# Kernel optimization log

Hardware: AMD Instinct MI355X
Metric: run time of the kernel (lower is better)

Reference implementation:

```python
import jax, jax.numpy as jnp
import numpy as np

KS = 2       # kernel_size (pad (0,1,0,1)+unfold only tiles to HxW for k=2)
L = 2        # num_attn_blocks
NH = 4       # n_heads
C = 128      # latent_dim
DH = C // NH
SCALE = 1.0 / float(np.sqrt(DH))


def _ln(x, eps=1e-6):
    m = jnp.mean(x, axis=-1, keepdims=True)
    v = jnp.var(x, axis=-1, keepdims=True)
    return (x - m) * jax.lax.rsqrt(v + eps)


def setup_inputs() -> dict:
    key = jax.random.key(0)
    ks = jax.random.split(key, 24)
    B, Hd, Wd, upf = 2, 64, 96, 2
    d = {
        'feat_map': jax.random.normal(ks[0], (B, C, Hd, Wd), jnp.float32),
        'feat_map_up': jax.random.normal(ks[1], (B, C, Hd * upf, Wd * upf), jnp.float32),
    }
    shapes = {'ctx_ln_b': (L, C), 'q_w': (L, C, C), 'q_b': (L, C), 'k_w': (L, C, C), 'k_b': (L, C),
              'v_w': (L, C, C), 'v_b': (L, C), 'o_w': (L, C, C), 'o_b': (L, C),
              'fc1_w': (L, C, 4 * C), 'fc1_b': (L, 4 * C), 'fc2_w': (L, 4 * C, C), 'fc2_b': (L, C),
              'out1_w': (3 * C, 3 * C), 'out1_b': (3 * C,), 'out2_w': (3 * C, 1), 'out2_b': (1,)}
    for i, (n, shp) in enumerate(shapes.items()):
        d[n] = jax.random.normal(ks[2 + i], shp, jnp.float32) * 0.02
    d['ctx_ln_g'] = jnp.ones((L, C), jnp.float32)
    d['upsample_factor'] = 2
    return d


def _forward(feat_map, feat_map_up, ctx_ln_g, ctx_ln_b, q_w, q_b, k_w, k_b, v_w, v_b,
             o_w, o_b, fc1_w, fc1_b, fc2_w, fc2_b, out1_w, out1_b, out2_w, out2_b, upf):
    B, _, Hd, Wd = feat_map.shape
    Hu, Wu = Hd * upf, Wd * upf
    N, K2 = B * Hu * Wu, KS * KS
    rh = jnp.minimum((jnp.arange(Hu) // upf)[:, None] + jnp.arange(KS)[None, :], Hd - 1)  # (Hu,KS)
    rw = jnp.minimum((jnp.arange(Wu) // upf)[:, None] + jnp.arange(KS)[None, :], Wd - 1)  # (Wu,KS)
    ctx = feat_map[:, :, rh][:, :, :, :, rw]                      # (B,C,Hu,KS,Wu,KS)
    ctx = jnp.transpose(ctx, (0, 2, 4, 3, 5, 1)).reshape(N, K2, C)  # (N,K2,C)
    # ALiBi bias: -L1(|up pixel coord - upf*down window coord|), separable in y/x
    dy = -jnp.abs(jnp.arange(Hu)[:, None] - rh * upf).astype(jnp.float32)  # (Hu,KS)
    dx = -jnp.abs(jnp.arange(Wu)[:, None] - rw * upf).astype(jnp.float32)  # (Wu,KS)
    cd = (dy[:, None, :, None] + dx[None, :, None, :]).reshape(Hu * Wu, K2)
    cd = jnp.tile(cd, (B, 1))                                     # (N,K2)
    x24 = 24.0 ** (1.0 / NH)
    slopes = 1.0 / x24 ** (jnp.arange(NH, dtype=jnp.float32) + 1.0)
    bias = slopes[None, :, None, None] * cd[:, None, None, :]     # (N,NH,1,K2)

    x = jnp.transpose(feat_map_up, (0, 2, 3, 1)).reshape(N, 1, C)
    for l in range(L):
        xn = _ln(x)
        cn = _ln(ctx, eps=1e-5) * ctx_ln_g[l] + ctx_ln_b[l]
        q = (xn @ q_w[l] + q_b[l]).reshape(N, 1, NH, DH).transpose(0, 2, 1, 3)
        k = (cn @ k_w[l] + k_b[l]).reshape(N, K2, NH, DH).transpose(0, 2, 1, 3)
        v = (cn @ v_w[l] + v_b[l]).reshape(N, K2, NH, DH).transpose(0, 2, 1, 3)
        sim = jnp.einsum('nhqd,nhkd->nhqk', q, k) * SCALE + bias
        attn = jax.nn.softmax(sim, axis=-1)
        o = jnp.einsum('nhqk,nhkd->nhqd', attn, v).transpose(0, 2, 1, 3).reshape(N, 1, C)
        x = x + o @ o_w[l] + o_b[l]
        h = _ln(x)
        x = x + jax.nn.gelu(h @ fc1_w[l] + fc1_b[l], approximate=True) @ fc2_w[l] + fc2_b[l]

    xf = _ln(x)      # (N,1,C)
    cf = _ln(ctx)    # (N,K2,C)
    fin = jnp.concatenate([jnp.broadcast_to(xf, (N, K2, C)), cf, xf - cf], axis=-1)  # (N,K2,3C)
    h1 = jax.nn.gelu(fin @ out1_w + out1_b, approximate=False)
    out = (h1 @ out2_w + out2_b).reshape(B, Hu, Wu, K2).transpose(0, 3, 1, 2)  # (B,K2,Hu,Wu)
    return jax.nn.softmax(out, axis=1)


def reference(feat_map, feat_map_up, ctx_ln_b, q_w, q_b, k_w, k_b, v_w, v_b, o_w, o_b,
              fc1_w, fc1_b, fc2_w, fc2_b, out1_w, out1_b, out2_w, out2_b, ctx_ln_g,
              upsample_factor):
    return _forward(feat_map, feat_map_up, ctx_ln_g, ctx_ln_b, q_w, q_b, k_w, k_b,
                    v_w, v_b, o_w, o_b, fc1_w, fc1_b, fc2_w, fc2_b,
                    out1_w, out1_b, out2_w, out2_b, upsample_factor)
```

## Files before the change

kernel.cpp:

```cpp
#include <hip/hip_runtime.h>
#include <math.h>

#define C_   128
#define HU_  128
#define WU_  192
#define HD_  64
#define WD_  96
#define HWD_ (HD_ * WD_)

typedef unsigned short u16;
typedef __attribute__((ext_vector_type(8))) short s8v;
typedef __attribute__((ext_vector_type(4))) float f4v;

#define OFF_Q   0
#define OFF_K   32768
#define OFF_V   65536
#define OFF_O   98304
#define OFF_F1  131072
#define OFF_F2  262144
#define OFF_XC  393216
#define OFF_CC  442368
#define OFF_NRM 491520
#define OFF_VB  2064384

#define SLOT 2176

__device__ __forceinline__ u16 f2bf(float f) {
    unsigned u = __float_as_uint(f);
    unsigned r = (u + 0x7FFFu + ((u >> 16) & 1u)) >> 16;
    return (u16)r;
}
__device__ __forceinline__ float bfu(u16 h) { return __uint_as_float(((unsigned)h) << 16); }

__device__ __forceinline__ float gelu_tanh(float x) {
    float u = 1.5957691216057308f * (x + 0.044715f * x * x * x);
    float e = __expf(u);
    float th = 1.0f - 2.0f / (1.0f + e);
    return 0.5f * x * (1.0f + th);
}
__device__ __forceinline__ float fast_erf(float x) {
    float z = fabsf(x);
    float t = 1.0f / (1.0f + 0.3275911f * z);
    float p = t * (0.254829592f + t * (-0.284496736f + t * (1.421413741f +
              t * (-1.453152027f + t * 1.061405429f))));
    float r = 1.0f - p * __expf(-z * z);
    return copysignf(r, x);
}
__device__ __forceinline__ float gelu_erf(float x) {
    return 0.5f * x * (1.0f + fast_erf(x * 0.7071067811865476f));
}

__device__ __forceinline__ void glds1(const u16* src, u16* dst, int lane) {
    __builtin_amdgcn_global_load_lds(
        (const __attribute__((address_space(1))) void*)(src + (size_t)lane * 8),
        (__attribute__((address_space(3))) void*)dst, 16, 0, 0);
}
#define GW4() do { asm volatile("s_waitcnt vmcnt(4)" ::: "memory"); __builtin_amdgcn_s_barrier(); } while (0)
#define GW3() do { asm volatile("s_waitcnt vmcnt(3)" ::: "memory"); __builtin_amdgcn_s_barrier(); } while (0)
#define GW0() do { asm volatile("s_waitcnt vmcnt(0)" ::: "memory"); __builtin_amdgcn_s_barrier(); } while (0)
#define BAR() __builtin_amdgcn_s_barrier()
#define WFENCE() asm volatile("s_waitcnt lgkmcnt(0)" ::: "memory")

__global__ __launch_bounds__(256) void swz_all(
    const float* __restrict__ q_w, const float* __restrict__ k_w,
    const float* __restrict__ v_w, const float* __restrict__ o_w,
    const float* __restrict__ f1w, const float* __restrict__ f2w,
    const float* __restrict__ o1w,
    const float* __restrict__ ctx_g, const float* __restrict__ ctx_b,
    const float* __restrict__ vb_in, u16* __restrict__ ws)
{
    int tid = blockIdx.x * 256 + threadIdx.x;
    int f = tid >> 6, lane = tid & 63;
    if (f >= 964) return;
    if (f >= 960) {
        int lf = f - 960;
        int ly = lf >> 1, col = (lf & 1) * 64 + lane;
        float s = vb_in[ly * 128 + col];
        const float* bp = ctx_b + ly * 128;
        const float* wp = v_w + (size_t)ly * 128 * 128 + col;
        for (int c = 0; c < 128; ++c) s += bp[c] * wp[(size_t)c * 128];
        ((float*)(ws + OFF_VB))[ly * 128 + col] = s;
        return;
    }
    int rq = 8 * (lane >> 4), cq = lane & 15;
    const float* src; const float* src2 = nullptr; float sgn = 1.f;
    int NT, N, dstoff, lf;
    bool scale_g = false;
    if (f < 64)       { src = q_w;  NT = 8;  N = 128; dstoff = OFF_Q;  lf = f; }
    else if (f < 128) { src = k_w;  NT = 8;  N = 128; dstoff = OFF_K;  lf = f - 64;  scale_g = true; }
    else if (f < 192) { src = v_w;  NT = 8;  N = 128; dstoff = OFF_V;  lf = f - 128; scale_g = true; }
    else if (f < 256) { src = o_w;  NT = 8;  N = 128; dstoff = OFF_O;  lf = f - 192; }
    else if (f < 512) { src = f1w;  NT = 32; N = 512; dstoff = OFF_F1; lf = f - 256; }
    else if (f < 768) { src = f2w;  NT = 8;  N = 128; dstoff = OFF_F2; lf = f - 512; }
    else if (f < 864) { src = o1w;             src2 = o1w + 256 * 384; sgn =  1.f;
                        NT = 24; N = 384; dstoff = OFF_XC; lf = f - 768; }
    else              { src = o1w + 128 * 384; src2 = o1w + 256 * 384; sgn = -1.f;
                        NT = 24; N = 384; dstoff = OFF_CC; lf = f - 864; }
    int kt = lf / NT, nt = lf - kt * NT;
    int row0 = kt * 32 + rq, col = nt * 16 + cq;
    s8v o;
#pragma unroll
    for (int j = 0; j < 8; ++j) {
        float v = src[(size_t)(row0 + j) * N + col];
        if (src2) v += sgn * src2[(size_t)(row0 + j) * N + col];
        if (scale_g) v *= ctx_g[row0 + j];
        o[j] = (short)f2bf(v);
    }
    *(s8v*)(ws + dstoff + (size_t)lf * 512 + (size_t)lane * 8) = o;
}

__global__ __launch_bounds__(256) void norm_kernel(const float* __restrict__ fm,
                                                   u16* __restrict__ dst) {
    int row = blockIdx.x;
    int b = row >> 6, y = row & 63;
    __shared__ float tile[128 * 97];
    __shared__ float smean[96], srst[96];
    for (int idx = threadIdx.x; idx < 128 * 96; idx += 256) {
        int c = idx / 96, w = idx - c * 96;
        tile[c * 97 + w] = fm[(((size_t)b * 128 + c) * 64 + y) * 96 + w];
    }
    __syncthreads();
    if (threadIdx.x < 96) {
        int w = threadIdx.x;
        float s = 0.f, ss = 0.f;
        for (int c = 0; c < 128; ++c) { float v = tile[c * 97 + w]; s += v; ss += v * v; }
        float mn = s * (1.f / 128.f);
        smean[w] = mn;
        srst[w]  = rsqrtf(ss * (1.f / 128.f) - mn * mn + 1e-5f);
    }
    __syncthreads();
    for (int idx = threadIdx.x; idx < 96 * 16; idx += 256) {
        int w = idx >> 4, cg = idx & 15;
        float mn = smean[w], iv = srst[w];
        s8v o;
#pragma unroll
        for (int j = 0; j < 8; ++j)
            o[j] = (short)f2bf((tile[(8 * cg + j) * 97 + w] - mn) * iv);
        *(s8v*)(dst + ((size_t)row * 96 + w) * 128 + 8 * cg) = o;
    }
}

__global__ __launch_bounds__(128, 2) void fused_kernel(
    const u16*  __restrict__ nrmb, const float* __restrict__ fmu,
    const u16*  __restrict__ wsb,
    const float* __restrict__ qb, const float* __restrict__ ob,
    const float* __restrict__ f1b, const float* __restrict__ f2b,
    const float* __restrict__ o1b, const float* __restrict__ o2w,
    const float* __restrict__ o2b,
    float* __restrict__ out)
{
    const int tid  = threadIdx.x;
    const int wid  = tid >> 6;
    const int lane = tid & 63;
    const int cidx = lane & 15, quad = lane >> 4;
    const int n0 = blockIdx.x * 32 + wid * 16;
    const int b  = n0 / (HU_ * WU_);
    const int rem = n0 - b * (HU_ * WU_);
    const int hu  = rem / WU_;
    const int wu0 = rem - hu * WU_;

    __shared__ __align__(16) u16 wlds[2][4096];
    __shared__ __align__(16) u16 arena2[2][2 * SLOT];
    __shared__ float s_at2[2][272];
    u16*   const arena = arena2[wid];
    float* const s_at  = s_at2[wid];
    float* const s_rs  = s_at;

    const float* vbp = (const float*)(wsb + OFF_VB);

    float xacc[8][4];
#pragma unroll
    for (int nt = 0; nt < 8; ++nt) {
        int ch = 16 * nt + cidx;
        float4 v = *(const float4*)(fmu + ((size_t)(b * C_ + ch) * HU_ + hu) * WU_ + wu0 + 4 * quad);
        xacc[nt][0] = v.x; xacc[nt][1] = v.y; xacc[nt][2] = v.z; xacc[nt][3] = v.w;
    }

    const float slopes[4] = {0.451801007f, 0.204124145f, 0.092223264f, 0.041666668f};
    const int ry0 = min(hu >> 1, HD_ - 1);
    const int ry1 = min((hu >> 1) + 1, HD_ - 1);
    const float dyv0 = -(float)abs(hu - 2 * ry0);
    const float dyv1 = -(float)abs(hu - 2 * ry1);

    const int k2l = cidx & 3;
    const int ryl = (k2l >> 1) ? ry1 : ry0;
    int cbase[4];
#pragma unroll
    for (int mt = 0; mt < 4; ++mt) {
        int p = 4 * mt + (cidx >> 2);
        int rxv = min(((wu0 + p) >> 1) + (k2l & 1), WD_ - 1);
        cbase[mt] = ((b * HD_ + ryl) * WD_ + rxv) * 128;
    }

#pragma unroll 1
    for (int ly = 0; ly < 2; ++ly) {
        const u16* Wq = wsb + OFF_Q  + ly * 16384;
        const u16* Wk = wsb + OFF_K  + ly * 16384;
        const u16* Wv = wsb + OFF_V  + ly * 16384;
        const u16* Wo = wsb + OFF_O  + ly * 16384;
        const u16* W1 = wsb + OFF_F1 + ly * 65536;
        const u16* W2 = wsb + OFF_F2 + ly * 65536;

        s8v fr[4][2];

#pragma unroll
        for (int jl = 0; jl < 4; ++jl) {
            int j = 4 * wid + jl;
            glds1(Wq + (size_t)j * 512, &wlds[0][j * 512], lane);
        }
#pragma unroll
        for (int jl = 0; jl < 4; ++jl) {
            int j = 4 * wid + jl;
            glds1(Wq + (size_t)(8 + j) * 512, &wlds[1][j * 512], lane);
        }

        {
            float mo[4], io[4];
#pragma unroll
            for (int r = 0; r < 4; ++r) {
                float s = 0.f, ss = 0.f;
#pragma unroll
                for (int nt = 0; nt < 8; ++nt) { float v = xacc[nt][r]; s += v; ss += v * v; }
#pragma unroll
                for (int m = 1; m <= 8; m <<= 1) { s += __shfl_xor(s, m, 64); ss += __shfl_xor(ss, m, 64); }
                float mn = s * (1.f / 128.f);
                mo[r] = mn; io[r] = rsqrtf(ss * (1.f / 128.f) - mn * mn + 1e-6f);
            }
#pragma unroll
            for (int nt = 0; nt < 8; ++nt)
#pragma unroll
                for (int r = 0; r < 4; ++r)
                    arena[(4 * quad + r) * 136 + 16 * nt + cidx] =
                        f2bf((xacc[nt][r] - mo[r]) * io[r]);
        }
        WFENCE();
        s8v a_xn[4];
#pragma unroll
        for (int kt = 0; kt < 4; ++kt)
            a_xn[kt] = *(const s8v*)(arena + cidx * 136 + kt * 32 + 8 * quad);

        {
            f4v qa[8];
#pragma unroll
            for (int nt = 0; nt < 8; ++nt) {
                float bvv = qb[ly * C_ + 16 * nt + cidx];
                f4v t = {bvv, bvv, bvv, bvv}; qa[nt] = t;
            }
#pragma unroll
            for (int g = 0; g < 4; ++g) {
                if (g < 3) { GW4(); } else { GW0(); }
#pragma unroll
                for (int nt = 0; nt < 8; ++nt) {
                    s8v w = *(const s8v*)&wlds[g & 1][nt * 512 + lane * 8];
                    qa[nt] = __builtin_amdgcn_mfma_f32_16x16x32_bf16(a_xn[g], w, qa[nt], 0, 0, 0);
                }
                BAR();
                if (g < 2) {
#pragma unroll
                    for (int jl = 0; jl < 4; ++jl) {
                        int j = 4 * wid + jl;
                        glds1(Wq + (size_t)((g + 2) * 8 + j) * 512, &wlds[g & 1][j * 512], lane);
                    }
                }
            }
#pragma unroll
            for (int kt = 0; kt < 4; ++kt)
#pragma unroll
                for (int i = 0; i < 2; ++i)
                    fr[kt][i] = *(const s8v*)(nrmb + cbase[i] + kt * 32 + 8 * quad);
#pragma unroll
            for (int jl = 0; jl < 4; ++jl) {
                int j = 4 * wid + jl;
                glds1(Wk + (size_t)(((j & 3) * 8) + (j >> 2)) * 512, &wlds[0][j * 512], lane);
            }
#pragma unroll
            for (int jl = 0; jl < 4; ++jl) {
                int j = 4 * wid + jl;
                int jc = 8 + j;
                glds1(Wk + (size_t)(((jc & 3) * 8) + (jc >> 2)) * 512, &wlds[1][j * 512], lane);
            }
#pragma unroll
            for (int nt = 0; nt < 8; ++nt)
#pragma unroll
                for (int r = 0; r < 4; ++r)
                    arena[(4 * quad + r) * 136 + 16 * nt + cidx] = f2bf(qa[nt][r]);
        }
        WFENCE();

#pragma unroll
        for (int g = 0; g < 8; ++g) {
            if (g < 7) { GW4(); } else { GW0(); }
            if (g == 4) {
#pragma unroll
                for (int kt = 0; kt < 4; ++kt)
#pragma unroll
                    for (int i = 0; i < 2; ++i)
                        fr[kt][i] = *(const s8v*)(nrmb + cbase[2 + i] + kt * 32 + 8 * quad);
            }
            const int mh = g >> 2, h = g & 3;
            float part[2][4];
#pragma unroll
            for (int i = 0; i < 2; ++i)
#pragma unroll
                for (int r = 0; r < 4; ++r) part[i][r] = 0.f;
#pragma unroll
            for (int ntp = 0; ntp < 2; ++ntp) {
                const int nt = 2 * h + ntp;
                f4v ka[2];
#pragma unroll
                for (int i = 0; i < 2; ++i) { f4v t = {0.f, 0.f, 0.f, 0.f}; ka[i] = t; }
#pragma unroll
                for (int kt = 0; kt < 4; ++kt) {
                    s8v w = *(const s8v*)&wlds[g & 1][(ntp * 4 + kt) * 512 + lane * 8];
                    ka[0] = __builtin_amdgcn_mfma_f32_16x16x32_bf16(fr[kt][0], w, ka[0], 0, 0, 0);
                    ka[1] = __builtin_amdgcn_mfma_f32_16x16x32_bf16(fr[kt][1], w, ka[1], 0, 0, 0);
                }
#pragma unroll
                for (int i = 0; i < 2; ++i) {
                    float qv = bfu(arena[(4 * (2 * mh + i) + quad) * 136 + 16 * nt + cidx]);
#pragma unroll
                    for (int r = 0; r < 4; ++r) part[i][r] = fmaf(qv, ka[i][r], part[i][r]);
                }
            }
#pragma unroll
            for (int i = 0; i < 2; ++i)
#pragma unroll
                for (int r = 0; r < 4; ++r) {
#pragma unroll
                    for (int m = 1; m <= 8; m <<= 1) part[i][r] += __shfl_xor(part[i][r], m, 64);
                }
            if (cidx == 0) {
#pragma unroll
                for (int i = 0; i < 2; ++i) {
                    float4 t = {part[i][0], part[i][1], part[i][2], part[i][3]};
                    *(float4*)&s_at[(4 * (2 * mh + i) + quad) * 16 + 4 * h] = t;
                }
            }
            BAR();
            if (g < 6) {
                const int gn = g + 2;
#pragma unroll
                for (int jl = 0; jl < 4; ++jl) {
                    int j = 4 * wid + jl;
                    int jc = 8 * (gn & 3) + j;
                    glds1(Wk + (size_t)(((jc & 3) * 8) + (jc >> 2)) * 512, &wlds[g & 1][j * 512], lane);
                }
            }
        }
#pragma unroll
        for (int kt = 0; kt < 4; ++kt)
#pragma unroll
            for (int i = 0; i < 2; ++i)
                fr[kt][i] = *(const s8v*)(nrmb + cbase[i] + kt * 32 + 8 * quad);
#pragma unroll
        for (int jl = 0; jl < 4; ++jl) {
            int j = 4 * wid + jl;
            glds1(Wv + (size_t)(((j & 3) * 8) + (j >> 2)) * 512, &wlds[0][j * 512], lane);
        }
#pragma unroll
        for (int jl = 0; jl < 4; ++jl) {
            int j = 4 * wid + jl;
            glds1(Wv + (size_t)(((j & 3) * 8) + 2 + (j >> 2)) * 512, &wlds[1][j * 512], lane);
        }
        WFENCE();

        {
            int p = lane >> 2, h = lane & 3;
            float4 sc = *(float4*)&s_at[p * 16 + 4 * h];
            int pw = wu0 + p;
            float sim[4] = {sc.x, sc.y, sc.z, sc.w};
#pragma unroll
            for (int r = 0; r < 4; ++r) {
                int rxv = min((pw >> 1) + (r & 1), WD_ - 1);
                float cd = ((r >> 1) ? dyv1 : dyv0) - (float)abs(pw - 2 * rxv);
                sim[r] = sim[r] * 0.17677669529663687f + slopes[h] * cd;
            }
            float mx = fmaxf(fmaxf(sim[0], sim[1]), fmaxf(sim[2], sim[3]));
            float e0 = __expf(sim[0] - mx), e1 = __expf(sim[1] - mx);
            float e2 = __expf(sim[2] - mx), e3 = __expf(sim[3] - mx);
            float si = 1.f / (e0 + e1 + e2 + e3);
            float4 at = {e0 * si, e1 * si, e2 * si, e3 * si};
            *(float4*)&s_at[p * 16 + 4 * h] = at;
        }
        WFENCE();

#pragma unroll
        for (int g = 0; g < 8; ++g) {
            if (g < 7) { GW4(); } else { GW0(); }
            if (g == 4) {
#pragma unroll
                for (int kt = 0; kt < 4; ++kt)
#pragma unroll
                    for (int i = 0; i < 2; ++i)
                        fr[kt][i] = *(const s8v*)(nrmb + cbase[2 + i] + kt * 32 + 8 * quad);
            }
            const int mh = g >> 2, gp = g & 3;
#pragma unroll
            for (int ntp = 0; ntp < 2; ++ntp) {
                const int nt = 2 * gp + ntp;
                float vbb = vbp[ly * C_ + 16 * nt + cidx];
                f4v va[2];
#pragma unroll
                for (int i = 0; i < 2; ++i) { f4v t = {vbb, vbb, vbb, vbb}; va[i] = t; }
#pragma unroll
                for (int kt = 0; kt < 4; ++kt) {
                    s8v w = *(const s8v*)&wlds[g & 1][(ntp * 4 + kt) * 512 + lane * 8];
                    va[0] = __builtin_amdgcn_mfma_f32_16x16x32_bf16(fr[kt][0], w, va[0], 0, 0, 0);
                    va[1] = __builtin_amdgcn_mfma_f32_16x16x32_bf16(fr[kt][1], w, va[1], 0, 0, 0);
                }
                const int h = nt >> 1;
#pragma unroll
                for (int i = 0; i < 2; ++i) {
                    const int mt = 2 * mh + i;
                    float4 at = *(float4*)&s_at[(4 * mt + quad) * 16 + 4 * h];
                    float ov = at.x * va[i][0] + at.y * va[i][1] + at.z * va[i][2] + at.w * va[i][3];
                    arena[(4 * mt + quad) * 136 + 16 * nt + cidx] = f2bf(ov);
                }
            }
            BAR();
            if (g < 6) {
                const int gq = (g + 2) & 3;
#pragma unroll
                for (int jl = 0; jl < 4; ++jl) {
                    int j = 4 * wid + jl;
                    glds1(Wv + (size_t)(((j & 3) * 8) + 2 * gq + (j >> 2)) * 512, &wlds[g & 1][j * 512], lane);
                }
            }
        }
#pragma unroll
        for (int jl = 0; jl < 4; ++jl) {
            int j = 4 * wid + jl;
            glds1(Wo + (size_t)j * 512, &wlds[0][j * 512], lane);
        }
#pragma unroll
        for (int jl = 0; jl < 4; ++jl) {
            int j = 4 * wid + jl;
            glds1(Wo + (size_t)(8 + j) * 512, &wlds[1][j * 512], lane);
        }
        WFENCE();

        {
            s8v a_o[4];
#pragma unroll
            for (int kt = 0; kt < 4; ++kt)
                a_o[kt] = *(const s8v*)(arena + cidx * 136 + kt * 32 + 8 * quad);
            f4v oa[8];
#pragma unroll
            for (int nt = 0; nt < 8; ++nt) {
                float bvv = ob[ly * C_ + 16 * nt + cidx];
                f4v t = {bvv, bvv, bvv, bvv}; oa[nt] = t;
            }
#pragma unroll
            for (int g = 0; g < 4; ++g) {
                if (g < 3) { GW4(); } else { GW0(); }
#pragma unroll
                for (int nt = 0; nt < 8; ++nt) {
                    s8v w = *(const s8v*)&wlds[g & 1][nt * 512 + lane * 8];
                    oa[nt] = __builtin_amdgcn_mfma_f32_16x16x32_bf16(a_o[g], w, oa[nt], 0, 0, 0);
                }
                BAR();
                if (g < 2) {
#pragma unroll
                    for (int jl = 0; jl < 4; ++jl) {
                        int j = 4 * wid + jl;
                        glds1(Wo + (size_t)((g + 2) * 8 + j) * 512, &wlds[g & 1][j * 512], lane);
                    }
                }
            }
#pragma unroll
            for (int jl = 0; jl < 4; ++jl) {
                int j = 4 * wid + jl;
                glds1(W1 + (size_t)j * 512, &wlds[0][j * 512], lane);
            }
#pragma unroll
            for (int jl = 0; jl < 4; ++jl) {
                int j = 4 * wid + jl;
                glds1(W1 + (size_t)(32 + j) * 512, &wlds[1][j * 512], lane);
            }
#pragma unroll
            for (int nt = 0; nt < 8; ++nt)
#pragma unroll
                for (int r = 0; r < 4; ++r) xacc[nt][r] += oa[nt][r];
        }

        {
            float mo[4], io[4];
#pragma unroll
            for (int r = 0; r < 4; ++r) {
                float s = 0.f, ss = 0.f;
#pragma unroll
                for (int nt = 0; nt < 8; ++nt) { float v = xacc[nt][r]; s += v; ss += v * v; }
#pragma unroll
                for (int m = 1; m <= 8; m <<= 1) { s += __shfl_xor(s, m, 64); ss += __shfl_xor(ss, m, 64); }
                float mn = s * (1.f / 128.f);
                mo[r] = mn; io[r] = rsqrtf(ss * (1.f / 128.f) - mn * mn + 1e-6f);
            }
#pragma unroll
            for (int nt = 0; nt < 8; ++nt)
#pragma unroll
                for (int r = 0; r < 4; ++r)
                    arena[(4 * quad + r) * 136 + 16 * nt + cidx] =
                        f2bf((xacc[nt][r] - mo[r]) * io[r]);
        }
        WFENCE();
        s8v a_hn[4];
#pragma unroll
        for (int kt = 0; kt < 4; ++kt)
            a_hn[kt] = *(const s8v*)(arena + cidx * 136 + kt * 32 + 8 * quad);

        {
            f4v ga[8];
#pragma unroll
            for (int nt = 0; nt < 8; ++nt) {
                float bvv = f2b[ly * C_ + 16 * nt + cidx];
                f4v t = {bvv, bvv, bvv, bvv}; ga[nt] = t;
            }
#pragma unroll 1
            for (int c = 0; c < 4; ++c) {
                f4v fa[8];
#pragma unroll
                for (int nt = 0; nt < 8; ++nt) {
                    float bvv = f1b[ly * 512 + 128 * c + 16 * nt + cidx];
                    f4v t = {bvv, bvv, bvv, bvv}; fa[nt] = t;
                }
#pragma unroll
                for (int g = 0; g < 4; ++g) {
                    if (g < 3) { GW4(); } else { GW0(); }
#pragma unroll
                    for (int nt = 0; nt < 8; ++nt) {
                        s8v w = *(const s8v*)&wlds[g & 1][nt * 512 + lane * 8];
                        fa[nt] = __builtin_amdgcn_mfma_f32_16x16x32_bf16(a_hn[g], w, fa[nt], 0, 0, 0);
                    }
                    BAR();
                    if (g < 2) {
#pragma unroll
                        for (int jl = 0; jl < 4; ++jl) {
                            int j = 4 * wid + jl;
                            glds1(W1 + (size_t)((g + 2) * 32 + 8 * c + j) * 512, &wlds[g & 1][j * 512], lane);
                        }
                    }
                }
#pragma unroll
                for (int jl = 0; jl < 4; ++jl) {
                    int j = 4 * wid + jl;
                    glds1(W2 + (size_t)(32 * c + j) * 512, &wlds[0][j * 512], lane);
                }
#pragma unroll
                for (int jl = 0; jl < 4; ++jl) {
                    int j = 4 * wid + jl;
                    glds1(W2 + (size_t)(32 * c + 8 + j) * 512, &wlds[1][j * 512], lane);
                }
#pragma unroll
                for (int nt = 0; nt < 8; ++nt)
#pragma unroll
                    for (int r = 0; r < 4; ++r)
                        arena[SLOT + (4 * quad + r) * 136 + 16 * nt + cidx] =
                            f2bf(gelu_tanh(fa[nt][r]));
                WFENCE();
#pragma unroll
                for (int g = 0; g < 4; ++g) {
                    if (g < 3) { GW4(); } else { GW0(); }
                    s8v a = *(const s8v*)(arena + SLOT + cidx * 136 + g * 32 + 8 * quad);
#pragma unroll
                    for (int nt = 0; nt < 8; ++nt) {
                        s8v w = *(const s8v*)&wlds[g & 1][nt * 512 + lane * 8];
                        ga[nt] = __builtin_amdgcn_mfma_f32_16x16x32_bf16(a, w, ga[nt], 0, 0, 0);
                    }
                    BAR();
                    if (g < 2) {
#pragma unroll
                        for (int jl = 0; jl < 4; ++jl) {
                            int j = 4 * wid + jl;
                            glds1(W2 + (size_t)(32 * c + (g + 2) * 8 + j) * 512, &wlds[g & 1][j * 512], lane);
                        }
                    }
                }
                if (c < 3) {
#pragma unroll
                    for (int jl = 0; jl < 4; ++jl) {
                        int j = 4 * wid + jl;
                        glds1(W1 + (size_t)(8 * (c + 1) + j) * 512, &wlds[0][j * 512], lane);
                    }
#pragma unroll
                    for (int jl = 0; jl < 4; ++jl) {
                        int j = 4 * wid + jl;
                        glds1(W1 + (size_t)(32 + 8 * (c + 1) + j) * 512, &wlds[1][j * 512], lane);
                    }
                }
            }
#pragma unroll
            for (int nt = 0; nt < 8; ++nt)
#pragma unroll
                for (int r = 0; r < 4; ++r) xacc[nt][r] += ga[nt][r];
        }
    }

    const u16* Wxc = wsb + OFF_XC;
    const u16* Wcc = wsb + OFF_CC;
#pragma unroll
    for (int jl = 0; jl < 3; ++jl) {
        int j = 3 * wid + jl;
        glds1(Wxc + (size_t)((j / 3) * 24 + (j % 3)) * 512, &wlds[0][j * 512], lane);
    }
#pragma unroll
    for (int jl = 0; jl < 3; ++jl) {
        int j = 3 * wid + jl;
        glds1(Wxc + (size_t)((2 + j / 3) * 24 + (j % 3)) * 512, &wlds[1][j * 512], lane);
    }
    {
        float mo[4], io[4];
#pragma unroll
        for (int r = 0; r < 4; ++r) {
            float s = 0.f, ss = 0.f;
#pragma unroll
            for (int nt = 0; nt < 8; ++nt) { float v = xacc[nt][r]; s += v; ss += v * v; }
#pragma unroll
            for (int m = 1; m <= 8; m <<= 1) { s += __shfl_xor(s, m, 64); ss += __shfl_xor(ss, m, 64); }
            float mn = s * (1.f / 128.f);
            mo[r] = mn; io[r] = rsqrtf(ss * (1.f / 128.f) - mn * mn + 1e-6f);
        }
#pragma unroll
        for (int nt = 0; nt < 8; ++nt)
#pragma unroll
            for (int r = 0; r < 4; ++r)
                arena[(4 * quad + r) * 136 + 16 * nt + cidx] =
                    f2bf((xacc[nt][r] - mo[r]) * io[r]);
    }
    WFENCE();
    s8v a_xf[4];
#pragma unroll
    for (int kt = 0; kt < 4; ++kt)
        a_xf[kt] = *(const s8v*)(arena + cidx * 136 + kt * 32 + 8 * quad);

    float part[4][4];
#pragma unroll
    for (int mt = 0; mt < 4; ++mt)
#pragma unroll
        for (int r = 0; r < 4; ++r) part[mt][r] = 0.f;

#pragma unroll 1
    for (int it = 0; it < 8; ++it) {
        const int nbase = 6 * (it >> 1) + 3 * (it & 1);
        {
            f4v hx[3];
#pragma unroll
            for (int ntl = 0; ntl < 3; ++ntl) {
                float hb = o1b[16 * (nbase + ntl) + cidx];
                f4v t = {hb, hb, hb, hb}; hx[ntl] = t;
            }
            GW3();
#pragma unroll
            for (int kt = 0; kt < 2; ++kt)
#pragma unroll
                for (int ntl = 0; ntl < 3; ++ntl) {
                    s8v w = *(const s8v*)&wlds[0][(kt * 3 + ntl) * 512 + lane * 8];
                    hx[ntl] = __builtin_amdgcn_mfma_f32_16x16x32_bf16(a_xf[kt], w, hx[ntl], 0, 0, 0);
                }
            GW0();
#pragma unroll
            for (int kt = 2; kt < 4; ++kt)
#pragma unroll
                for (int ntl = 0; ntl < 3; ++ntl) {
                    s8v w = *(const s8v*)&wlds[1][((kt - 2) * 3 + ntl) * 512 + lane * 8];
                    hx[ntl] = __builtin_amdgcn_mfma_f32_16x16x32_bf16(a_xf[kt], w, hx[ntl], 0, 0, 0);
                }
            BAR();
            if (it < 7) {
                const int nb2 = 6 * ((it + 1) >> 1) + 3 * ((it + 1) & 1);
#pragma unroll
                for (int jl = 0; jl < 3; ++jl) {
                    int j = 3 * wid + jl;
                    glds1(Wxc + (size_t)((j / 3) * 24 + nb2 + (j % 3)) * 512, &wlds[0][j * 512], lane);
                }
#pragma unroll
                for (int jl = 0; jl < 3; ++jl) {
                    int j = 3 * wid + jl;
                    glds1(Wxc + (size_t)((2 + j / 3) * 24 + nb2 + (j % 3)) * 512, &wlds[1][j * 512], lane);
                }
            }
#pragma unroll
            for (int ntl = 0; ntl < 3; ++ntl)
#pragma unroll
                for (int r = 0; r < 4; ++r)
                    arena[SLOT + (4 * quad + r) * 56 + 16 * ntl + cidx] = f2bf(hx[ntl][r]);
        }
        WFENCE();

        f4v hc[3][4];
#pragma unroll
        for (int ntl = 0; ntl < 3; ++ntl)
#pragma unroll
            for (int mt = 0; mt < 4; ++mt) { f4v t = {0.f, 0.f, 0.f, 0.f}; hc[ntl][mt] = t; }
#pragma unroll 1
        for (int kt = 0; kt < 4; ++kt) {
            s8v frh[4];
#pragma unroll
            for (int mt = 0; mt < 4; ++mt)
                frh[mt] = *(const s8v*)(nrmb + cbase[mt] + kt * 32 + 8 * quad);
#pragma unroll
            for (int ntl = 0; ntl < 3; ++ntl) {
                s8v w = *(const s8v*)(Wcc + ((size_t)((kt * 24 + nbase + ntl) * 64 + lane)) * 8);
#pragma unroll
                for (int mt = 0; mt < 4; ++mt)
                    hc[ntl][mt] = __builtin_amdgcn_mfma_f32_16x16x32_bf16(frh[mt], w, hc[ntl][mt], 0, 0, 0);
            }
        }

#pragma unroll
        for (int ntl = 0; ntl < 3; ++ntl) {
            float w2v = o2w[16 * (nbase + ntl) + cidx];
#pragma unroll
            for (int mt = 0; mt < 4; ++mt)
#pragma unroll
                for (int r = 0; r < 4; ++r) {
                    float h1 = hc[ntl][mt][r] +
                               bfu(arena[SLOT + (4 * mt + quad) * 56 + 16 * ntl + cidx]);
                    part[mt][r] = fmaf(gelu_erf(h1), w2v, part[mt][r]);
                }
        }
        WFENCE();
    }

#pragma unroll
    for (int mt = 0; mt < 4; ++mt)
#pragma unroll
        for (int r = 0; r < 4; ++r) {
#pragma unroll
            for (int m = 1; m <= 8; m <<= 1) part[mt][r] += __shfl_xor(part[mt][r], m, 64);
            part[mt][r] += o2b[0];
        }
    if (cidx == 0) {
#pragma unroll
        for (int mt = 0; mt < 4; ++mt) {
            float4 t = {part[mt][0], part[mt][1], part[mt][2], part[mt][3]};
            *(float4*)&s_rs[(4 * mt + quad) * 4] = t;
        }
    }
    WFENCE();

    if (lane < 16) {
        int p = lane;
        float4 vv = *(float4*)&s_rs[4 * p];
        float mx = fmaxf(fmaxf(vv.x, vv.y), fmaxf(vv.z, vv.w));
        float e0 = __expf(vv.x - mx), e1 = __expf(vv.y - mx);
        float e2 = __expf(vv.z - mx), e3 = __expf(vv.w - mx);
        float si = 1.f / (e0 + e1 + e2 + e3);
        size_t base = ((size_t)(b * 4) * HU_ + hu) * WU_ + wu0 + p;
        out[base]                          = e0 * si;
        out[base + (size_t)HU_ * WU_]      = e1 * si;
        out[base + (size_t)2 * HU_ * WU_]  = e2 * si;
        out[base + (size_t)3 * HU_ * WU_]  = e3 * si;
    }
}

extern "C" void kernel_launch(void* const* d_in, const int* in_sizes, int n_in,
                              void* d_out, int out_size, void* d_ws, size_t ws_size,
                              hipStream_t stream) {
    const float* feat_map    = (const float*)d_in[0];
    const float* feat_map_up = (const float*)d_in[1];
    const float* ctx_ln_b    = (const float*)d_in[2];
    const float* q_w  = (const float*)d_in[3];
    const float* q_b  = (const float*)d_in[4];
    const float* k_w  = (const float*)d_in[5];
    const float* v_w  = (const float*)d_in[7];
    const float* v_b  = (const float*)d_in[8];
    const float* o_w  = (const float*)d_in[9];
    const float* o_b  = (const float*)d_in[10];
    const float* fc1_w = (const float*)d_in[11];
    const float* fc1_b = (const float*)d_in[12];
    const float* fc2_w = (const float*)d_in[13];
    const float* fc2_b = (const float*)d_in[14];
    const float* out1_w = (const float*)d_in[15];
    const float* out1_b = (const float*)d_in[16];
    const float* out2_w = (const float*)d_in[17];
    const float* out2_b = (const float*)d_in[18];
    const float* ctx_ln_g = (const float*)d_in[19];
    float* out = (float*)d_out;
    u16* ws = (u16*)d_ws;

    swz_all<<<242, 256, 0, stream>>>(q_w, k_w, v_w, o_w, fc1_w, fc2_w, out1_w,
                                     ctx_ln_g, ctx_ln_b, v_b, ws);
    norm_kernel<<<128, 256, 0, stream>>>(feat_map, ws + OFF_NRM);

    fused_kernel<<<1536, 128, 0, stream>>>(
        ws + OFF_NRM, feat_map_up, ws,
        q_b, o_b, fc1_b, fc2_b,
        out1_b, out2_w, out2_b, out);
}
```

Measured before the change: 412.6 us.

## Widen fused kernel to four waves per block sharing LDS weight tiles

The fused kernel moves from 2 to 4 waves per block (256 threads, half as many blocks), so each weight chunk staged through global_load_lds is shared by 64 rows instead of 32. Each wave now issues half as many async loads per chunk, and the vmcnt waits are adjusted to match. The per-wave attention scratch is folded into the arena to save LDS, and the reload of the second half of the context fragments is moved earlier in the K/V loops. In exchange, barriers now synchronise four waves, which can add stall time, and register pressure under launch_bounds(256,2) may limit occupancy.

```diff
diff --git a/kernel.cpp b/kernel.cpp
--- a/kernel.cpp
+++ b/kernel.cpp
@@ -55,8 +55,7 @@
         (const __attribute__((address_space(1))) void*)(src + (size_t)lane * 8),
         (__attribute__((address_space(3))) void*)dst, 16, 0, 0);
 }
-#define GW4() do { asm volatile("s_waitcnt vmcnt(4)" ::: "memory"); __builtin_amdgcn_s_barrier(); } while (0)
-#define GW3() do { asm volatile("s_waitcnt vmcnt(3)" ::: "memory"); __builtin_amdgcn_s_barrier(); } while (0)
+#define GW2() do { asm volatile("s_waitcnt vmcnt(2)" ::: "memory"); __builtin_amdgcn_s_barrier(); } while (0)
 #define GW0() do { asm volatile("s_waitcnt vmcnt(0)" ::: "memory"); __builtin_amdgcn_s_barrier(); } while (0)
 #define BAR() __builtin_amdgcn_s_barrier()
 #define WFENCE() asm volatile("s_waitcnt lgkmcnt(0)" ::: "memory")
@@ -140,7 +139,7 @@
     }
 }
 
-__global__ __launch_bounds__(128, 2) void fused_kernel(
+__global__ __launch_bounds__(256, 2) void fused_kernel(
     const u16*  __restrict__ nrmb, const float* __restrict__ fmu,
     const u16*  __restrict__ wsb,
     const float* __restrict__ qb, const float* __restrict__ ob,
@@ -153,17 +152,16 @@
     const int wid  = tid >> 6;
     const int lane = tid & 63;
     const int cidx = lane & 15, quad = lane >> 4;
-    const int n0 = blockIdx.x * 32 + wid * 16;
+    const int n0 = blockIdx.x * 64 + wid * 16;
     const int b  = n0 / (HU_ * WU_);
     const int rem = n0 - b * (HU_ * WU_);
     const int hu  = rem / WU_;
     const int wu0 = rem - hu * WU_;
 
     __shared__ __align__(16) u16 wlds[2][4096];
-    __shared__ __align__(16) u16 arena2[2][2 * SLOT];
-    __shared__ float s_at2[2][272];
+    __shared__ __align__(16) u16 arena2[4][2 * SLOT];
     u16*   const arena = arena2[wid];
-    float* const s_at  = s_at2[wid];
+    float* const s_at  = (float*)(arena + SLOT + 1024);
     float* const s_rs  = s_at;
 
     const float* vbp = (const float*)(wsb + OFF_VB);
@@ -204,13 +202,13 @@
         s8v fr[4][2];
 
 #pragma unroll
-        for (int jl = 0; jl < 4; ++jl) {
-            int j = 4 * wid + jl;
+        for (int jl = 0; jl < 2; ++jl) {
+            int j = 2 * wid + jl;
             glds1(Wq + (size_t)j * 512, &wlds[0][j * 512], lane);
         }
 #pragma unroll
-        for (int jl = 0; jl < 4; ++jl) {
-            int j = 4 * wid + jl;
+        for (int jl = 0; jl < 2; ++jl) {
+            int j = 2 * wid + jl;
             glds1(Wq + (size_t)(8 + j) * 512, &wlds[1][j * 512], lane);
         }
 
@@ -248,7 +246,7 @@
             }
 #pragma unroll
             for (int g = 0; g < 4; ++g) {
-                if (g < 3) { GW4(); } else { GW0(); }
+                if (g < 3) { GW2(); } else { GW0(); }
 #pragma unroll
                 for (int nt = 0; nt < 8; ++nt) {
                     s8v w = *(const s8v*)&wlds[g & 1][nt * 512 + lane * 8];
@@ -257,8 +255,8 @@
                 BAR();
                 if (g < 2) {
 #pragma unroll
-                    for (int jl = 0; jl < 4; ++jl) {
-                        int j = 4 * wid + jl;
+                    for (int jl = 0; jl < 2; ++jl) {
+                        int j = 2 * wid + jl;
                         glds1(Wq + (size_t)((g + 2) * 8 + j) * 512, &wlds[g & 1][j * 512], lane);
                     }
                 }
@@ -269,13 +267,13 @@
                 for (int i = 0; i < 2; ++i)
                     fr[kt][i] = *(const s8v*)(nrmb + cbase[i] + kt * 32 + 8 * quad);
 #pragma unroll
-            for (int jl = 0; jl < 4; ++jl) {
-                int j = 4 * wid + jl;
+            for (int jl = 0; jl < 2; ++jl) {
+                int j = 2 * wid + jl;
                 glds1(Wk + (size_t)(((j & 3) * 8) + (j >> 2)) * 512, &wlds[0][j * 512], lane);
             }
 #pragma unroll
-            for (int jl = 0; jl < 4; ++jl) {
-                int j = 4 * wid + jl;
+            for (int jl = 0; jl < 2; ++jl) {
+                int j = 2 * wid + jl;
                 int jc = 8 + j;
                 glds1(Wk + (size_t)(((jc & 3) * 8) + (jc >> 2)) * 512, &wlds[1][j * 512], lane);
             }
@@ -289,14 +287,7 @@
 
 #pragma unroll
         for (int g = 0; g < 8; ++g) {
-            if (g < 7) { GW4(); } else { GW0(); }
-            if (g == 4) {
-#pragma unroll
-                for (int kt = 0; kt < 4; ++kt)
-#pragma unroll
-                    for (int i = 0; i < 2; ++i)
-                        fr[kt][i] = *(const s8v*)(nrmb + cbase[2 + i] + kt * 32 + 8 * quad);
-            }
+            if (g < 7) { GW2(); } else { GW0(); }
             const int mh = g >> 2, h = g & 3;
             float part[2][4];
 #pragma unroll
@@ -337,11 +328,18 @@
                 }
             }
             BAR();
+            if (g == 2) {
+#pragma unroll
+                for (int kt = 0; kt < 4; ++kt)
+#pragma unroll
+                    for (int i = 0; i < 2; ++i)
+                        fr[kt][i] = *(const s8v*)(nrmb + cbase[2 + i] + kt * 32 + 8 * quad);
+            }
             if (g < 6) {
                 const int gn = g + 2;
 #pragma unroll
-                for (int jl = 0; jl < 4; ++jl) {
-                    int j = 4 * wid + jl;
+                for (int jl = 0; jl < 2; ++jl) {
+                    int j = 2 * wid + jl;
                     int jc = 8 * (gn & 3) + j;
                     glds1(Wk + (size_t)(((jc & 3) * 8) + (jc >> 2)) * 512, &wlds[g & 1][j * 512], lane);
                 }
@@ -353,13 +351,13 @@
             for (int i = 0; i < 2; ++i)
                 fr[kt][i] = *(const s8v*)(nrmb + cbase[i] + kt * 32 + 8 * quad);
 #pragma unroll
-        for (int jl = 0; jl < 4; ++jl) {
-            int j = 4 * wid + jl;
+        for (int jl = 0; jl < 2; ++jl) {
+            int j = 2 * wid + jl;
             glds1(Wv + (size_t)(((j & 3) * 8) + (j >> 2)) * 512, &wlds[0][j * 512], lane);
         }
 #pragma unroll
-        for (int jl = 0; jl < 4; ++jl) {
-            int j = 4 * wid + jl;
+        for (int jl = 0; jl < 2; ++jl) {
+            int j = 2 * wid + jl;
             glds1(Wv + (size_t)(((j & 3) * 8) + 2 + (j >> 2)) * 512, &wlds[1][j * 512], lane);
         }
         WFENCE();
@@ -386,14 +384,7 @@
 
 #pragma unroll
         for (int g = 0; g < 8; ++g) {
-            if (g < 7) { GW4(); } else { GW0(); }
-            if (g == 4) {
-#pragma unroll
-                for (int kt = 0; kt < 4; ++kt)
-#pragma unroll
-                    for (int i = 0; i < 2; ++i)
-                        fr[kt][i] = *(const s8v*)(nrmb + cbase[2 + i] + kt * 32 + 8 * quad);
-            }
+            if (g < 7) { GW2(); } else { GW0(); }
             const int mh = g >> 2, gp = g & 3;
 #pragma unroll
             for (int ntp = 0; ntp < 2; ++ntp) {
@@ -418,23 +409,30 @@
                 }
             }
             BAR();
+            if (g == 2) {
+#pragma unroll
+                for (int kt = 0; kt < 4; ++kt)
+#pragma unroll
+                    for (int i = 0; i < 2; ++i)
+                        fr[kt][i] = *(const s8v*)(nrmb + cbase[2 + i] + kt * 32 + 8 * quad);
+            }
             if (g < 6) {
                 const int gq = (g + 2) & 3;
 #pragma unroll
-                for (int jl = 0; jl < 4; ++jl) {
-                    int j = 4 * wid + jl;
+                for (int jl = 0; jl < 2; ++jl) {
+                    int j = 2 * wid + jl;
                     glds1(Wv + (size_t)(((j & 3) * 8) + 2 * gq + (j >> 2)) * 512, &wlds[g & 1][j * 512], lane);
                 }
             }
         }
 #pragma unroll
-        for (int jl = 0; jl < 4; ++jl) {
-            int j = 4 * wid + jl;
+        for (int jl = 0; jl < 2; ++jl) {
+            int j = 2 * wid + jl;
             glds1(Wo + (size_t)j * 512, &wlds[0][j * 512], lane);
         }
 #pragma unroll
-        for (int jl = 0; jl < 4; ++jl) {
-            int j = 4 * wid + jl;
+        for (int jl = 0; jl < 2; ++jl) {
+            int j = 2 * wid + jl;
             glds1(Wo + (size_t)(8 + j) * 512, &wlds[1][j * 512], lane);
         }
         WFENCE();
@@ -452,7 +450,7 @@
             }
 #pragma unroll
             for (int g = 0; g < 4; ++g) {
-                if (g < 3) { GW4(); } else { GW0(); }
+                if (g < 3) { GW2(); } else { GW0(); }
 #pragma unroll
                 for (int nt = 0; nt < 8; ++nt) {
                     s8v w = *(const s8v*)&wlds[g & 1][nt * 512 + lane * 8];
@@ -461,20 +459,20 @@
                 BAR();
                 if (g < 2) {
 #pragma unroll
-                    for (int jl = 0; jl < 4; ++jl) {
-                        int j = 4 * wid + jl;
+                    for (int jl = 0; jl < 2; ++jl) {
+                        int j = 2 * wid + jl;
                         glds1(Wo + (size_t)((g + 2) * 8 + j) * 512, &wlds[g & 1][j * 512], lane);
                     }
                 }
             }
 #pragma unroll
-            for (int jl = 0; jl < 4; ++jl) {
-                int j = 4 * wid + jl;
+            for (int jl = 0; jl < 2; ++jl) {
+                int j = 2 * wid + jl;
                 glds1(W1 + (size_t)j * 512, &wlds[0][j * 512], lane);
             }
 #pragma unroll
-            for (int jl = 0; jl < 4; ++jl) {
-                int j = 4 * wid + jl;
+            for (int jl = 0; jl < 2; ++jl) {
+                int j = 2 * wid + jl;
                 glds1(W1 + (size_t)(32 + j) * 512, &wlds[1][j * 512], lane);
             }
 #pragma unroll
@@ -525,7 +523,7 @@
                 }
 #pragma unroll
                 for (int g = 0; g < 4; ++g) {
-                    if (g < 3) { GW4(); } else { GW0(); }
+                    if (g < 3) { GW2(); } else { GW0(); }
 #pragma unroll
                     for (int nt = 0; nt < 8; ++nt) {
                         s8v w = *(const s8v*)&wlds[g & 1][nt * 512 + lane * 8];
@@ -534,20 +532,20 @@
                     BAR();
                     if (g < 2) {
 #pragma unroll
-                        for (int jl = 0; jl < 4; ++jl) {
-                            int j = 4 * wid + jl;
+                        for (int jl = 0; jl < 2; ++jl) {
+                            int j = 2 * wid + jl;
                             glds1(W1 + (size_t)((g + 2) * 32 + 8 * c + j) * 512, &wlds[g & 1][j * 512], lane);
                         }
                     }
                 }
 #pragma unroll
-                for (int jl = 0; jl < 4; ++jl) {
-                    int j = 4 * wid + jl;
+                for (int jl = 0; jl < 2; ++jl) {
+                    int j = 2 * wid + jl;
                     glds1(W2 + (size_t)(32 * c + j) * 512, &wlds[0][j * 512], lane);
                 }
 #pragma unroll
-                for (int jl = 0; jl < 4; ++jl) {
-                    int j = 4 * wid + jl;
+                for (int jl = 0; jl < 2; ++jl) {
+                    int j = 2 * wid + jl;
                     glds1(W2 + (size_t)(32 * c + 8 + j) * 512, &wlds[1][j * 512], lane);
                 }
 #pragma unroll
@@ -559,7 +557,7 @@
                 WFENCE();
 #pragma unroll
                 for (int g = 0; g < 4; ++g) {
-                    if (g < 3) { GW4(); } else { GW0(); }
+                    if (g < 3) { GW2(); } else { GW0(); }
                     s8v a = *(const s8v*)(arena + SLOT + cidx * 136 + g * 32 + 8 * quad);
 #pragma unroll
                     for (int nt = 0; nt < 8; ++nt) {
@@ -569,21 +567,21 @@
                     BAR();
                     if (g < 2) {
 #pragma unroll
-                        for (int jl = 0; jl < 4; ++jl) {
-                            int j = 4 * wid + jl;
+                        for (int jl = 0; jl < 2; ++jl) {
+                            int j = 2 * wid + jl;
                             glds1(W2 + (size_t)(32 * c + (g + 2) * 8 + j) * 512, &wlds[g & 1][j * 512], lane);
                         }
                     }
                 }
                 if (c < 3) {
 #pragma unroll
-                    for (int jl = 0; jl < 4; ++jl) {
-                        int j = 4 * wid + jl;
+                    for (int jl = 0; jl < 2; ++jl) {
+                        int j = 2 * wid + jl;
                         glds1(W1 + (size_t)(8 * (c + 1) + j) * 512, &wlds[0][j * 512], lane);
                     }
 #pragma unroll
-                    for (int jl = 0; jl < 4; ++jl) {
-                        int j = 4 * wid + jl;
+                    for (int jl = 0; jl < 2; ++jl) {
+                        int j = 2 * wid + jl;
                         glds1(W1 + (size_t)(32 + 8 * (c + 1) + j) * 512, &wlds[1][j * 512], lane);
                     }
                 }
@@ -600,12 +598,7 @@
 #pragma unroll
     for (int jl = 0; jl < 3; ++jl) {
         int j = 3 * wid + jl;
-        glds1(Wxc + (size_t)((j / 3) * 24 + (j % 3)) * 512, &wlds[0][j * 512], lane);
-    }
-#pragma unroll
-    for (int jl = 0; jl < 3; ++jl) {
-        int j = 3 * wid + jl;
-        glds1(Wxc + (size_t)((2 + j / 3) * 24 + (j % 3)) * 512, &wlds[1][j * 512], lane);
+        glds1(Wxc + (size_t)((j / 3) * 24 + (j % 3)) * 512, &wlds[j / 6][(j % 6) * 512], lane);
     }
     {
         float mo[4], io[4];
@@ -648,7 +641,8 @@
                 float hb = o1b[16 * (nbase + ntl) + cidx];
                 f4v t = {hb, hb, hb, hb}; hx[ntl] = t;
             }
-            GW3();
+            if (wid < 2) { asm volatile("s_waitcnt vmcnt(0)" ::: "memory"); }
+            BAR();
 #pragma unroll
             for (int kt = 0; kt < 2; ++kt)
 #pragma unroll
@@ -656,7 +650,8 @@
                     s8v w = *(const s8v*)&wlds[0][(kt * 3 + ntl) * 512 + lane * 8];
                     hx[ntl] = __builtin_amdgcn_mfma_f32_16x16x32_bf16(a_xf[kt], w, hx[ntl], 0, 0, 0);
                 }
-            GW0();
+            if (wid >= 2) { asm volatile("s_waitcnt vmcnt(0)" ::: "memory"); }
+            BAR();
 #pragma unroll
             for (int kt = 2; kt < 4; ++kt)
 #pragma unroll
@@ -670,12 +665,7 @@
 #pragma unroll
                 for (int jl = 0; jl < 3; ++jl) {
                     int j = 3 * wid + jl;
-                    glds1(Wxc + (size_t)((j / 3) * 24 + nb2 + (j % 3)) * 512, &wlds[0][j * 512], lane);
-                }
-#pragma unroll
-                for (int jl = 0; jl < 3; ++jl) {
-                    int j = 3 * wid + jl;
-                    glds1(Wxc + (size_t)((2 + j / 3) * 24 + nb2 + (j % 3)) * 512, &wlds[1][j * 512], lane);
+                    glds1(Wxc + (size_t)((j / 3) * 24 + nb2 + (j % 3)) * 512, &wlds[j / 6][(j % 6) * 512], lane);
                 }
             }
 #pragma unroll
@@ -782,7 +772,7 @@
                                      ctx_ln_g, ctx_ln_b, v_b, ws);
     norm_kernel<<<128, 256, 0, stream>>>(feat_map, ws + OFF_NRM);
 
-    fused_kernel<<<1536, 128, 0, stream>>>(
+    fused_kernel<<<768, 256, 0, stream>>>(
         ws + OFF_NRM, feat_map_up, ws,
         q_b, o_b, fc1_b, fc2_b,
         out1_b, out2_w, out2_b, out);
```

Result: no change. 407.5 us (-1.2%).
